# Optimization experiments

Measured on AMD Instinct MI355X. Metric: run time of the kernel, lower is better.

Reference implementation:

```python
import jax, jax.numpy as jnp
import numpy as np

N_ENT = 50000
N_REL = 200
DIM = 128
N_BASES = 4
NUM_RELATIONS = 2 * N_REL  # RGCNConv num_relations
E = 200000
S = 20000


def rgcn_conv(x, edge_index, edge_type, edge_norm, basis, att, root, bias, n_nodes):
    """RGCNConv with basis decomposition, aggr='mean'.
    x: [N, Din]; basis: [B, Din, Dout]; att: [R, B]; root: [Din, Dout]; bias: [Dout].
    """
    src, dst = edge_index[0], edge_index[1]
    x_j = x[src]                      # [E, Din] gather
    att_e = att[edge_type]            # [E, B]
    # message: x_j @ (att_e @ basis) without materializing per-edge [Din,Dout] weights
    msg = jnp.einsum('ei,bio,eb->eo', x_j, basis, att_e)  # [E, Dout]
    msg = msg * edge_norm[:, None]
    agg = jax.ops.segment_sum(msg, dst, num_segments=n_nodes)            # [N, Dout]
    cnt = jax.ops.segment_sum(jnp.ones_like(edge_norm), dst, num_segments=n_nodes)
    agg = agg / jnp.maximum(cnt, 1.0)[:, None]            # mean aggregation
    return agg + x @ root + bias


def setup_inputs() -> dict:
    key = jax.random.key(0)
    ks = jax.random.split(key, 20)
    d = {}
    d['entity'] = jnp.arange(N_ENT, dtype=jnp.int64) if jax.config.read('jax_enable_x64') else jnp.arange(N_ENT, dtype=jnp.int32)
    d['edge_index'] = jax.random.randint(ks[0], (2, E), 0, N_ENT)
    d['edge_type'] = jax.random.randint(ks[1], (E,), 0, NUM_RELATIONS)
    d['edge_norm'] = jax.random.uniform(ks[2], (E,), dtype=jnp.float32)
    d['samples'] = jax.random.randint(ks[3], (S, 3), 0, N_REL)
    d['DAD_rel'] = jax.random.normal(ks[4], (N_REL, N_REL), dtype=jnp.float32) * 0.05
    # learned parameters
    d['entity_emb'] = jax.random.normal(ks[5], (N_ENT, DIM), dtype=jnp.float32) * 0.02
    d['relation_emb'] = jax.random.normal(ks[6], (N_REL, DIM), dtype=jnp.float32) * 0.02
    d['entity_context_tab'] = jax.random.normal(ks[7], (N_ENT, DIM), dtype=jnp.float32) * 0.02
    d['relation_context_tab'] = jax.random.normal(ks[8], (N_REL, DIM), dtype=jnp.float32) * 0.02
    d['relation_gcn_weight'] = jax.random.normal(ks[9], (DIM, DIM), dtype=jnp.float32) * 0.02
    d['gate_entity'] = jax.random.uniform(ks[10], (DIM,), dtype=jnp.float32)
    d['gate_relation'] = jax.random.uniform(ks[11], (DIM,), dtype=jnp.float32)
    d['basis1'] = jax.random.normal(ks[12], (N_BASES, DIM, DIM), dtype=jnp.float32) * 0.02
    d['att1'] = jax.random.normal(ks[13], (NUM_RELATIONS, N_BASES), dtype=jnp.float32) * 0.1
    d['root1'] = jax.random.normal(ks[14], (DIM, DIM), dtype=jnp.float32) * 0.02
    d['bias1'] = jnp.zeros((DIM,), dtype=jnp.float32)
    d['basis2'] = jax.random.normal(ks[15], (N_BASES, DIM, DIM), dtype=jnp.float32) * 0.02
    d['att2'] = jax.random.normal(ks[16], (NUM_RELATIONS, N_BASES), dtype=jnp.float32) * 0.1
    d['root2'] = jax.random.normal(ks[17], (DIM, DIM), dtype=jnp.float32) * 0.02
    d['bias2'] = jnp.zeros((DIM,), dtype=jnp.float32)
    return d


def reference(entity, edge_index, edge_type, edge_norm, samples, DAD_rel,
              entity_emb, relation_emb, entity_context_tab, relation_context_tab,
              relation_gcn_weight, gate_entity, gate_relation,
              basis1, att1, root1, bias1, basis2, att2, root2, bias2):
    n_nodes = entity.shape[0]
    ent_ctx = entity_context_tab[entity]                  # [N, D]
    rel_ctx = relation_context_tab                        # arange over all relations -> full table
    ent_ctx = jax.nn.relu(rgcn_conv(ent_ctx, edge_index, edge_type, edge_norm,
                                    basis1, att1, root1, bias1, n_nodes))
    ent_ctx = jax.nn.relu(rgcn_conv(ent_ctx, edge_index, edge_type, edge_norm,
                                    basis2, att2, root2, bias2, n_nodes))
    rel_ctx = jax.nn.relu((DAD_rel @ rel_ctx) @ relation_gcn_weight)
    ge = jax.nn.sigmoid(gate_entity)
    gr = jax.nn.sigmoid(gate_relation)
    h, r, t = samples[:, 0], samples[:, 1], samples[:, 2]
    head_o = ge * entity_emb[h] + (1.0 - ge) * ent_ctx[h]
    rel_o = gr * relation_emb[r] + (1.0 - gr) * rel_ctx[r]
    tail_o = ge * entity_emb[t] + (1.0 - ge) * ent_ctx[t]
    return jnp.stack([head_o, rel_o, tail_o])             # [3, S, D]
```

## Files before the change

kernel.cpp:

```cpp
#include <hip/hip_runtime.h>
#include <hip/hip_bf16.h>

typedef short s8v  __attribute__((ext_vector_type(8)));
typedef float f16v __attribute__((ext_vector_type(16)));

__device__ __forceinline__ unsigned short f2bf(float x) {
    unsigned u = __float_as_uint(x);
    unsigned r = ((u >> 16) & 1u) + 0x7FFFu;
    return (unsigned short)((u + r) >> 16);
}
__device__ __forceinline__ float bf2f(unsigned short h) {
    return __uint_as_float(((unsigned)h) << 16);
}

__global__ __launch_bounds__(256) void hist_kernel(
    const int* __restrict__ edge_index, int* __restrict__ deg, int E)
{
    int e = blockIdx.x * 256 + threadIdx.x;
    if (e < E) atomicAdd(&deg[edge_index[E + e]], 1);
}

__global__ __launch_bounds__(1024) void scanA_kernel(
    const int* __restrict__ deg, int* __restrict__ row_start,
    int* __restrict__ btot, int N)
{
    __shared__ int wtot[16];
    __shared__ int woff[16];
    const int tid = threadIdx.x, lane = tid & 63, wid = tid >> 6;
    int i = blockIdx.x * 1024 + tid;
    int v = (i < N) ? deg[i] : 0;
    int x = v;
    #pragma unroll
    for (int d = 1; d < 64; d <<= 1) {
        int t = __shfl_up(x, d, 64);
        if (lane >= d) x += t;
    }
    if (lane == 63) wtot[wid] = x;
    __syncthreads();
    if (wid == 0 && lane < 16) {
        int s = wtot[lane];
        int y = s;
        #pragma unroll
        for (int d = 1; d < 16; d <<= 1) {
            int t = __shfl_up(y, d, 16);
            if (lane >= d) y += t;
        }
        woff[lane] = y - s;
        if (lane == 15) btot[blockIdx.x] = y;
    }
    __syncthreads();
    if (i < N) row_start[i] = woff[wid] + (x - v);
}

__global__ __launch_bounds__(1024) void scanC_kernel(
    int* __restrict__ row_start, int* __restrict__ cursor,
    const int* __restrict__ btot, int nB, int N)
{
    __shared__ int incl[64];
    const int tid = threadIdx.x;
    if (tid < 64) {
        int v = (tid < nB) ? btot[tid] : 0;
        int x = v;
        #pragma unroll
        for (int d = 1; d < 64; d <<= 1) {
            int t = __shfl_up(x, d, 64);
            if (tid >= d) x += t;
        }
        incl[tid] = x;
    }
    __syncthreads();
    int off = (blockIdx.x == 0) ? 0 : incl[blockIdx.x - 1];
    int i = blockIdx.x * 1024 + tid;
    if (i < N) {
        int r = row_start[i] + off;
        row_start[i] = r;
        cursor[i]    = r;
    }
    if (blockIdx.x == (unsigned)(nB - 1) && tid == 0)
        row_start[N] = incl[nB - 1];
}

__global__ __launch_bounds__(256) void mega_kernel(
    const float* __restrict__ DAD, const float* __restrict__ rtab,
    const float* __restrict__ Wrel, float* __restrict__ Rc, int NR,
    const int* __restrict__ edge_index, const int* __restrict__ edge_type,
    const float* __restrict__ edge_norm, int* __restrict__ cursor,
    const float* __restrict__ att1, const float* __restrict__ att2,
    int* __restrict__ src_s, float4* __restrict__ an1, float4* __restrict__ an2, int E,
    const float* __restrict__ tab, const int* __restrict__ entity,
    unsigned short* __restrict__ X0h, unsigned short* __restrict__ X0l, int N,
    const float* __restrict__ basis1, const float* __restrict__ root1,
    const float* __restrict__ basis2, const float* __restrict__ root2,
    unsigned short* __restrict__ Bp1h, unsigned short* __restrict__ Bp2h,
    int c1, int c2, int c3)
{
    __shared__ float smem[384];
    const int b = blockIdx.x, tid = threadIdx.x;

    if (b < c1) {
        float* part = smem;
        float* r1s  = smem + 256;
        int r = b;
        int o = tid & 127, q = tid >> 7;
        float s = 0.f;
        for (int j = q; j < NR; j += 2)
            s = fmaf(DAD[r * NR + j], rtab[j * 128 + o], s);
        part[q * 128 + o] = s;
        __syncthreads();
        if (tid < 128) r1s[tid] = part[tid] + part[128 + tid];
        __syncthreads();
        float s2 = 0.f;
        #pragma unroll 8
        for (int k = q * 64; k < q * 64 + 64; ++k)
            s2 = fmaf(r1s[k], Wrel[k * 128 + o], s2);
        part[q * 128 + o] = s2;
        __syncthreads();
        if (tid < 128)
            Rc[r * 128 + tid] = fmaxf(part[tid] + part[128 + tid], 0.f);
    } else if (b < c2) {
        int e = (b - c1) * 256 + tid;
        if (e >= E) return;
        int dst = edge_index[E + e];
        int et  = edge_type[e];
        float n = edge_norm[e];
        int pos = atomicAdd(&cursor[dst], 1);
        src_s[pos] = edge_index[e];
        float4 a1 = *(const float4*)&att1[(size_t)et * 4];
        float4 a2 = *(const float4*)&att2[(size_t)et * 4];
        an1[pos] = make_float4(n * a1.x, n * a1.y, n * a1.z, n * a1.w);
        an2[pos] = make_float4(n * a2.x, n * a2.y, n * a2.z, n * a2.w);
    } else if (b < c3) {
        int idx = (b - c2) * 256 + tid;
        int nn = idx >> 4, part = idx & 15;
        if (nn < N) {
            int src = entity[nn];
            const float4* sp = (const float4*)&tab[(size_t)src * 128 + part * 8];
            float4 v0 = sp[0], v1 = sp[1];
            float vs[8] = {v0.x, v0.y, v0.z, v0.w, v1.x, v1.y, v1.z, v1.w};
            s8v h8, l8;
            #pragma unroll
            for (int j = 0; j < 8; ++j) {
                unsigned short h = f2bf(vs[j]);
                h8[j] = (short)h;
                l8[j] = (short)f2bf(vs[j] - bf2f(h));
            }
            *(s8v*)&X0h[(size_t)nn * 128 + part * 8] = h8;
            *(s8v*)&X0l[(size_t)nn * 128 + part * 8] = l8;
        }
    } else {
        int bb = b - c3;
        int layer = bb >= 320;
        int idx = (layer ? bb - 320 : bb) * 256 + tid;
        int n = idx & 127, k = idx >> 7;
        const float* basis = layer ? basis2 : basis1;
        const float* root  = layer ? root2  : root1;
        float v = (k < 512) ? basis[((k & 3) << 14) + ((k >> 2) << 7) + n]
                            : root[((k - 512) << 7) + n];
        size_t pos = (((size_t)(k >> 3) * 128) + n) * 8 + (k & 7);
        (layer ? Bp2h : Bp1h)[pos] = f2bf(v);
    }
}

__global__ __launch_bounds__(512, 4) void layer_kernel(
    const unsigned short* __restrict__ Xh,
    const unsigned short* __restrict__ Xl,
    const int* __restrict__ row_start,
    const int* __restrict__ src_s,
    const float4* __restrict__ an,
    const unsigned short* __restrict__ Bph,
    const float* __restrict__ bias,
    unsigned short* __restrict__ Xoh,
    unsigned short* __restrict__ Xol,
    int N)
{
    __shared__ unsigned short Whi[64 * 32 * 8];

    const int tid   = threadIdx.x;
    const int node0 = blockIdx.x * 32;

    {
        const int g = tid >> 4, l = tid & 15;
        const int gn = node0 + g;
        const bool ok = gn < N;
        int s0 = ok ? row_start[gn] : 0;
        int s1 = ok ? row_start[gn + 1] : 0;
        float acc[8][4];
        #pragma unroll
        for (int d = 0; d < 8; ++d)
            #pragma unroll
            for (int c = 0; c < 4; ++c) acc[d][c] = 0.f;

        const int se = s1 - 1;
        for (int q0 = s0; q0 < s1; q0 += 4) {
            int q1 = min(q0 + 1, se);
            int q2 = min(q0 + 2, se);
            int q3 = min(q0 + 3, se);
            int sA = src_s[q0], sB = src_s[q1];
            int sC = src_s[q2], sD = src_s[q3];
            float4 aA = an[q0], aB = an[q1];
            float4 aC = an[q2], aD = an[q3];
            if (q0 + 1 > se) aB = make_float4(0.f, 0.f, 0.f, 0.f);
            if (q0 + 2 > se) aC = make_float4(0.f, 0.f, 0.f, 0.f);
            if (q0 + 3 > se) aD = make_float4(0.f, 0.f, 0.f, 0.f);
            s8v hA = *(const s8v*)&Xh[(size_t)sA * 128 + (l << 3)];
            s8v hB = *(const s8v*)&Xh[(size_t)sB * 128 + (l << 3)];
            s8v hC = *(const s8v*)&Xh[(size_t)sC * 128 + (l << 3)];
            s8v hD = *(const s8v*)&Xh[(size_t)sD * 128 + (l << 3)];
            #pragma unroll
            for (int d = 0; d < 8; ++d) {
                float xA = bf2f((unsigned short)hA[d]);
                float xB = bf2f((unsigned short)hB[d]);
                float xC = bf2f((unsigned short)hC[d]);
                float xD = bf2f((unsigned short)hD[d]);
                acc[d][0] = fmaf(aA.x, xA, fmaf(aB.x, xB, fmaf(aC.x, xC, fmaf(aD.x, xD, acc[d][0]))));
                acc[d][1] = fmaf(aA.y, xA, fmaf(aB.y, xB, fmaf(aC.y, xC, fmaf(aD.y, xD, acc[d][1]))));
                acc[d][2] = fmaf(aA.z, xA, fmaf(aB.z, xB, fmaf(aC.z, xC, fmaf(aD.z, xD, acc[d][2]))));
                acc[d][3] = fmaf(aA.w, xA, fmaf(aB.w, xB, fmaf(aC.w, xC, fmaf(aD.w, xD, acc[d][3]))));
            }
        }
        float inv = 1.0f / fmaxf((float)(s1 - s0), 1.0f);
        #pragma unroll
        for (int f = 0; f < 4; ++f) {
            int kh   = 4 * l + f;
            int slot = g ^ (kh & 31);
            s8v h8;
            #pragma unroll
            for (int j = 0; j < 4; ++j) {
                h8[j]     = (short)f2bf(acc[2 * f][j]     * inv);
                h8[4 + j] = (short)f2bf(acc[2 * f + 1][j] * inv);
            }
            *(s8v*)&Whi[(kh * 32 + slot) * 8] = h8;
        }
    }

    const int lane = tid & 63, wv = tid >> 6;
    const int m    = lane & 31;
    const int kh8  = lane >> 5;
    s8v xh[8], xl[8];
    if (tid < 256) {
        const s8v z8 = {0, 0, 0, 0, 0, 0, 0, 0};
        int gn  = node0 + m;
        bool ok = gn < N;
        size_t xbase = (size_t)(ok ? gn : 0) * 128;
        #pragma unroll
        for (int q = 0; q < 8; ++q) {
            int dk = 2 * q + kh8;
            xh[q] = *(const s8v*)&Xh[xbase + dk * 8];
            xl[q] = *(const s8v*)&Xl[xbase + dk * 8];
        }
        if (!ok) {
            #pragma unroll
            for (int q = 0; q < 8; ++q) { xh[q] = z8; xl[q] = z8; }
        }
    }
    __syncthreads();
    if (tid >= 256) return;

    const int c0 = wv << 5;

    f16v acc;
    #pragma unroll
    for (int i = 0; i < 16; ++i) acc[i] = 0.f;

    s8v Bb[2][4];
    auto khg_of = [&](int t) {
        return (t < 8) ? (64 + 2 * t + kh8) : (2 * (t - 8) + kh8);
    };
    auto loadB4 = [&](int g, int buf) {
        #pragma unroll
        for (int q = 0; q < 4; ++q) {
            int khg = khg_of(g * 4 + q);
            size_t off = ((size_t)khg * 128 + c0 + m) * 8;
            Bb[buf][q] = *(const s8v*)&Bph[off];
        }
    };
    loadB4(0, 0);

    #pragma unroll
    for (int g = 0; g < 10; ++g) {
        int buf = g & 1;
        if (g < 9) loadB4(g + 1, buf ^ 1);
        #pragma unroll
        for (int q = 0; q < 4; ++q) {
            int t = g * 4 + q;
            if (t < 8) {
                acc = __builtin_amdgcn_mfma_f32_32x32x16_bf16(xl[t], Bb[buf][q], acc, 0, 0, 0);
                acc = __builtin_amdgcn_mfma_f32_32x32x16_bf16(xh[t], Bb[buf][q], acc, 0, 0, 0);
            } else {
                int khg  = 2 * (t - 8) + kh8;
                int slot = m ^ (khg & 31);
                s8v aH = *(const s8v*)&Whi[(khg * 32 + slot) * 8];
                acc = __builtin_amdgcn_mfma_f32_32x32x16_bf16(aH, Bb[buf][q], acc, 0, 0, 0);
            }
        }
    }

    int gc = c0 + m;
    float bv = bias[gc];
    const int rbase = kh8 << 2;
    #pragma unroll
    for (int reg = 0; reg < 16; ++reg) {
        int gr = node0 + rbase + (reg & 3) + ((reg >> 2) << 3);
        if (gr < N) {
            float v = fmaxf(acc[reg] + bv, 0.f);
            unsigned short h = f2bf(v);
            Xoh[(size_t)gr * 128 + gc] = h;
            Xol[(size_t)gr * 128 + gc] = f2bf(v - bf2f(h));
        }
    }
}

__global__ __launch_bounds__(256) void output_kernel(
    const int* __restrict__ samples,
    const float* __restrict__ gate_e,
    const float* __restrict__ gate_r,
    const float* __restrict__ ent_emb,
    const float* __restrict__ rel_emb,
    const unsigned short* __restrict__ ctx2h,
    const unsigned short* __restrict__ ctx2l,
    const float* __restrict__ relctx,
    float* __restrict__ out, int S)
{
    const int p   = blockIdx.y;
    const int o   = threadIdx.x & 127;
    const int sub = threadIdx.x >> 7;
    const float g = (p == 1) ? 1.0f / (1.0f + __expf(-gate_r[o]))
                             : 1.0f / (1.0f + __expf(-gate_e[o]));
    const int s0 = blockIdx.x * 8 + sub;
    #pragma unroll
    for (int k = 0; k < 4; ++k) {
        int s = s0 + k * 2;
        if (s >= S) break;
        float v;
        if (p == 1) {
            int idx = samples[s * 3 + 1];
            v = g * rel_emb[idx * 128 + o] + (1.0f - g) * relctx[idx * 128 + o];
        } else {
            int idx = samples[s * 3 + (p == 0 ? 0 : 2)];
            float c = bf2f(ctx2h[(size_t)idx * 128 + o]) + bf2f(ctx2l[(size_t)idx * 128 + o]);
            v = g * ent_emb[(size_t)idx * 128 + o] + (1.0f - g) * c;
        }
        out[(size_t)p * S * 128 + (size_t)s * 128 + o] = v;
    }
}

extern "C" void kernel_launch(void* const* d_in, const int* in_sizes, int n_in,
                              void* d_out, int out_size, void* d_ws, size_t ws_size,
                              hipStream_t stream)
{
    const int*   entity     = (const int*)d_in[0];
    const int*   edge_index = (const int*)d_in[1];
    const int*   edge_type  = (const int*)d_in[2];
    const float* edge_norm  = (const float*)d_in[3];
    const int*   samples    = (const int*)d_in[4];
    const float* DAD        = (const float*)d_in[5];
    const float* ent_emb    = (const float*)d_in[6];
    const float* rel_emb    = (const float*)d_in[7];
    const float* ent_tab    = (const float*)d_in[8];
    const float* rel_tab    = (const float*)d_in[9];
    const float* Wrel       = (const float*)d_in[10];
    const float* gate_e     = (const float*)d_in[11];
    const float* gate_r     = (const float*)d_in[12];
    const float* basis1     = (const float*)d_in[13];
    const float* att1       = (const float*)d_in[14];
    const float* root1      = (const float*)d_in[15];
    const float* bias1      = (const float*)d_in[16];
    const float* basis2     = (const float*)d_in[17];
    const float* att2       = (const float*)d_in[18];
    const float* root2      = (const float*)d_in[19];
    const float* bias2      = (const float*)d_in[20];

    const int N  = in_sizes[0];
    const int E  = in_sizes[2];
    const int S  = in_sizes[4] / 3;
    const int NR = in_sizes[9] / 128;

    unsigned short* X0h = (unsigned short*)d_ws;
    unsigned short* X0l = X0h + (size_t)N * 128;
    unsigned short* X1h = X0l + (size_t)N * 128;
    unsigned short* X1l = X1h + (size_t)N * 128;
    float4* an1    = (float4*)(X1l + (size_t)N * 128);
    float4* an2    = an1 + (E + 4);
    float* Rc      = (float*)(an2 + (E + 4));
    int*   deg     = (int*)(Rc + (size_t)NR * 128);
    int*   rstart  = deg + N;
    int*   cursor  = rstart + N + 1;
    int*   src_s   = cursor + N;
    int*   btot    = src_s + E + 4;
    int*   boff    = btot + 64;
    uintptr_t bt   = ((uintptr_t)(boff + 64) + 15) & ~(uintptr_t)15;
    unsigned short* Bp1h = (unsigned short*)bt;
    unsigned short* Bp2h = Bp1h + 80 * 128 * 8;

    const int egrid = (E + 255) / 256;
    const int lgrid = (N + 31) / 32;
    const int nB    = (N + 1023) / 1024;
    const int x0blocks = (N * 16 + 255) / 256;
    const int c1 = NR;
    const int c2 = c1 + egrid;
    const int c3 = c2 + x0blocks;
    const int mgrid = c3 + 640;

    hipMemsetAsync(deg, 0, (size_t)N * sizeof(int), stream);
    hist_kernel<<<egrid, 256, 0, stream>>>(edge_index, deg, E);
    scanA_kernel<<<nB, 1024, 0, stream>>>(deg, rstart, btot, N);
    scanC_kernel<<<nB, 1024, 0, stream>>>(rstart, cursor, btot, nB, N);
    mega_kernel<<<mgrid, 256, 0, stream>>>(
        DAD, rel_tab, Wrel, Rc, NR,
        edge_index, edge_type, edge_norm, cursor, att1, att2, src_s, an1, an2, E,
        ent_tab, entity, X0h, X0l, N,
        basis1, root1, basis2, root2, Bp1h, Bp2h,
        c1, c2, c3);

    layer_kernel<<<lgrid, 512, 0, stream>>>(X0h, X0l, rstart, src_s, an1,
                                            Bp1h, bias1, X1h, X1l, N);
    layer_kernel<<<lgrid, 512, 0, stream>>>(X1h, X1l, rstart, src_s, an2,
                                            Bp2h, bias2, X0h, X0l, N);

    output_kernel<<<dim3((S + 7) / 8, 3), 256, 0, stream>>>(
        samples, gate_e, gate_r, ent_emb, rel_emb, X0h, X0l, Rc, (float*)d_out, S);
}
```

Baseline: 295.1 us.

## Fuse entity-context gather into layer 1 and pack per-edge records

Drops the separate pass that gathered the entity context table into bf16 hi/lo X0 buffers. The first layer now reads fp32 rows straight from the table through entity[] and splits them in registers. Per-edge src, entity id, type and norm are packed into one int4 record, replacing the src_s array and two precomputed float4 attention arrays. Attention coefficients are now looked up and multiplied per edge inside each layer, which adds small gathers and FLOPs. Layer 1 reads fp32 neighbour rows, twice the bytes of bf16, in exchange for skipping the write and read of X0.

```diff
diff --git a/kernel.cpp b/kernel.cpp
--- a/kernel.cpp
+++ b/kernel.cpp
@@ -84,15 +84,12 @@
     const float* __restrict__ DAD, const float* __restrict__ rtab,
     const float* __restrict__ Wrel, float* __restrict__ Rc, int NR,
     const int* __restrict__ edge_index, const int* __restrict__ edge_type,
-    const float* __restrict__ edge_norm, int* __restrict__ cursor,
-    const float* __restrict__ att1, const float* __restrict__ att2,
-    int* __restrict__ src_s, float4* __restrict__ an1, float4* __restrict__ an2, int E,
-    const float* __restrict__ tab, const int* __restrict__ entity,
-    unsigned short* __restrict__ X0h, unsigned short* __restrict__ X0l, int N,
+    const float* __restrict__ edge_norm, const int* __restrict__ entity,
+    int* __restrict__ cursor, int4* __restrict__ rec, int E,
     const float* __restrict__ basis1, const float* __restrict__ root1,
     const float* __restrict__ basis2, const float* __restrict__ root2,
     unsigned short* __restrict__ Bp1h, unsigned short* __restrict__ Bp2h,
-    int c1, int c2, int c3)
+    int c1, int c2)
 {
     __shared__ float smem[384];
     const int b = blockIdx.x, tid = threadIdx.x;
@@ -123,32 +120,12 @@
         int dst = edge_index[E + e];
         int et  = edge_type[e];
         float n = edge_norm[e];
+        int src = edge_index[e];
+        int ent = entity[src];
         int pos = atomicAdd(&cursor[dst], 1);
-        src_s[pos] = edge_index[e];
-        float4 a1 = *(const float4*)&att1[(size_t)et * 4];
-        float4 a2 = *(const float4*)&att2[(size_t)et * 4];
-        an1[pos] = make_float4(n * a1.x, n * a1.y, n * a1.z, n * a1.w);
-        an2[pos] = make_float4(n * a2.x, n * a2.y, n * a2.z, n * a2.w);
-    } else if (b < c3) {
-        int idx = (b - c2) * 256 + tid;
-        int nn = idx >> 4, part = idx & 15;
-        if (nn < N) {
-            int src = entity[nn];
-            const float4* sp = (const float4*)&tab[(size_t)src * 128 + part * 8];
-            float4 v0 = sp[0], v1 = sp[1];
-            float vs[8] = {v0.x, v0.y, v0.z, v0.w, v1.x, v1.y, v1.z, v1.w};
-            s8v h8, l8;
-            #pragma unroll
-            for (int j = 0; j < 8; ++j) {
-                unsigned short h = f2bf(vs[j]);
-                h8[j] = (short)h;
-                l8[j] = (short)f2bf(vs[j] - bf2f(h));
-            }
-            *(s8v*)&X0h[(size_t)nn * 128 + part * 8] = h8;
-            *(s8v*)&X0l[(size_t)nn * 128 + part * 8] = l8;
-        }
+        rec[pos] = make_int4(src, ent, et, __float_as_int(n));
     } else {
-        int bb = b - c3;
+        int bb = b - c2;
         int layer = bb >= 320;
         int idx = (layer ? bb - 320 : bb) * 256 + tid;
         int n = idx & 127, k = idx >> 7;
@@ -161,12 +138,15 @@
     }
 }
 
+template<bool F32SRC>
 __global__ __launch_bounds__(512, 4) void layer_kernel(
     const unsigned short* __restrict__ Xh,
     const unsigned short* __restrict__ Xl,
+    const float* __restrict__ Xf,
+    const int* __restrict__ entity,
     const int* __restrict__ row_start,
-    const int* __restrict__ src_s,
-    const float4* __restrict__ an,
+    const int4* __restrict__ rec,
+    const float* __restrict__ att,
     const unsigned short* __restrict__ Bph,
     const float* __restrict__ bias,
     unsigned short* __restrict__ Xoh,
@@ -195,27 +175,58 @@
             int q1 = min(q0 + 1, se);
             int q2 = min(q0 + 2, se);
             int q3 = min(q0 + 3, se);
-            int sA = src_s[q0], sB = src_s[q1];
-            int sC = src_s[q2], sD = src_s[q3];
-            float4 aA = an[q0], aB = an[q1];
-            float4 aC = an[q2], aD = an[q3];
-            if (q0 + 1 > se) aB = make_float4(0.f, 0.f, 0.f, 0.f);
-            if (q0 + 2 > se) aC = make_float4(0.f, 0.f, 0.f, 0.f);
-            if (q0 + 3 > se) aD = make_float4(0.f, 0.f, 0.f, 0.f);
-            s8v hA = *(const s8v*)&Xh[(size_t)sA * 128 + (l << 3)];
-            s8v hB = *(const s8v*)&Xh[(size_t)sB * 128 + (l << 3)];
-            s8v hC = *(const s8v*)&Xh[(size_t)sC * 128 + (l << 3)];
-            s8v hD = *(const s8v*)&Xh[(size_t)sD * 128 + (l << 3)];
+            int4 rA = rec[q0], rB = rec[q1], rC = rec[q2], rD = rec[q3];
+            float4 tA = *(const float4*)&att[(size_t)rA.z * 4];
+            float4 tB = *(const float4*)&att[(size_t)rB.z * 4];
+            float4 tC = *(const float4*)&att[(size_t)rC.z * 4];
+            float4 tD = *(const float4*)&att[(size_t)rD.z * 4];
+            float nA = __int_as_float(rA.w), nB_ = __int_as_float(rB.w);
+            float nC = __int_as_float(rC.w), nD = __int_as_float(rD.w);
+            if (q0 + 1 > se) nB_ = 0.f;
+            if (q0 + 2 > se) nC = 0.f;
+            if (q0 + 3 > se) nD = 0.f;
+            float4 aA = make_float4(nA * tA.x, nA * tA.y, nA * tA.z, nA * tA.w);
+            float4 aB = make_float4(nB_ * tB.x, nB_ * tB.y, nB_ * tB.z, nB_ * tB.w);
+            float4 aC = make_float4(nC * tC.x, nC * tC.y, nC * tC.z, nC * tC.w);
+            float4 aD = make_float4(nD * tD.x, nD * tD.y, nD * tD.z, nD * tD.w);
+
+            float xA[8], xB[8], xC[8], xD[8];
+            if constexpr (F32SRC) {
+                const float4* pA = (const float4*)&Xf[(size_t)rA.y * 128 + (l << 3)];
+                const float4* pB = (const float4*)&Xf[(size_t)rB.y * 128 + (l << 3)];
+                const float4* pC = (const float4*)&Xf[(size_t)rC.y * 128 + (l << 3)];
+                const float4* pD = (const float4*)&Xf[(size_t)rD.y * 128 + (l << 3)];
+                float4 uA0 = pA[0], uA1 = pA[1];
+                float4 uB0 = pB[0], uB1 = pB[1];
+                float4 uC0 = pC[0], uC1 = pC[1];
+                float4 uD0 = pD[0], uD1 = pD[1];
+                xA[0]=uA0.x; xA[1]=uA0.y; xA[2]=uA0.z; xA[3]=uA0.w;
+                xA[4]=uA1.x; xA[5]=uA1.y; xA[6]=uA1.z; xA[7]=uA1.w;
+                xB[0]=uB0.x; xB[1]=uB0.y; xB[2]=uB0.z; xB[3]=uB0.w;
+                xB[4]=uB1.x; xB[5]=uB1.y; xB[6]=uB1.z; xB[7]=uB1.w;
+                xC[0]=uC0.x; xC[1]=uC0.y; xC[2]=uC0.z; xC[3]=uC0.w;
+                xC[4]=uC1.x; xC[5]=uC1.y; xC[6]=uC1.z; xC[7]=uC1.w;
+                xD[0]=uD0.x; xD[1]=uD0.y; xD[2]=uD0.z; xD[3]=uD0.w;
+                xD[4]=uD1.x; xD[5]=uD1.y; xD[6]=uD1.z; xD[7]=uD1.w;
+            } else {
+                s8v hA = *(const s8v*)&Xh[(size_t)rA.x * 128 + (l << 3)];
+                s8v hB = *(const s8v*)&Xh[(size_t)rB.x * 128 + (l << 3)];
+                s8v hC = *(const s8v*)&Xh[(size_t)rC.x * 128 + (l << 3)];
+                s8v hD = *(const s8v*)&Xh[(size_t)rD.x * 128 + (l << 3)];
+                #pragma unroll
+                for (int d = 0; d < 8; ++d) {
+                    xA[d] = bf2f((unsigned short)hA[d]);
+                    xB[d] = bf2f((unsigned short)hB[d]);
+                    xC[d] = bf2f((unsigned short)hC[d]);
+                    xD[d] = bf2f((unsigned short)hD[d]);
+                }
+            }
             #pragma unroll
             for (int d = 0; d < 8; ++d) {
-                float xA = bf2f((unsigned short)hA[d]);
-                float xB = bf2f((unsigned short)hB[d]);
-                float xC = bf2f((unsigned short)hC[d]);
-                float xD = bf2f((unsigned short)hD[d]);
-                acc[d][0] = fmaf(aA.x, xA, fmaf(aB.x, xB, fmaf(aC.x, xC, fmaf(aD.x, xD, acc[d][0]))));
-                acc[d][1] = fmaf(aA.y, xA, fmaf(aB.y, xB, fmaf(aC.y, xC, fmaf(aD.y, xD, acc[d][1]))));
-                acc[d][2] = fmaf(aA.z, xA, fmaf(aB.z, xB, fmaf(aC.z, xC, fmaf(aD.z, xD, acc[d][2]))));
-                acc[d][3] = fmaf(aA.w, xA, fmaf(aB.w, xB, fmaf(aC.w, xC, fmaf(aD.w, xD, acc[d][3]))));
+                acc[d][0] = fmaf(aA.x, xA[d], fmaf(aB.x, xB[d], fmaf(aC.x, xC[d], fmaf(aD.x, xD[d], acc[d][0]))));
+                acc[d][1] = fmaf(aA.y, xA[d], fmaf(aB.y, xB[d], fmaf(aC.y, xC[d], fmaf(aD.y, xD[d], acc[d][1]))));
+                acc[d][2] = fmaf(aA.z, xA[d], fmaf(aB.z, xB[d], fmaf(aC.z, xC[d], fmaf(aD.z, xD[d], acc[d][2]))));
+                acc[d][3] = fmaf(aA.w, xA[d], fmaf(aB.w, xB[d], fmaf(aC.w, xC[d], fmaf(aD.w, xD[d], acc[d][3]))));
             }
         }
         float inv = 1.0f / fmaxf((float)(s1 - s0), 1.0f);
@@ -241,12 +252,32 @@
         const s8v z8 = {0, 0, 0, 0, 0, 0, 0, 0};
         int gn  = node0 + m;
         bool ok = gn < N;
-        size_t xbase = (size_t)(ok ? gn : 0) * 128;
-        #pragma unroll
-        for (int q = 0; q < 8; ++q) {
-            int dk = 2 * q + kh8;
-            xh[q] = *(const s8v*)&Xh[xbase + dk * 8];
-            xl[q] = *(const s8v*)&Xl[xbase + dk * 8];
+        if constexpr (F32SRC) {
+            int en = ok ? entity[gn] : 0;
+            const float* base = &Xf[(size_t)en * 128];
+            #pragma unroll
+            for (int q = 0; q < 8; ++q) {
+                int dk = 2 * q + kh8;
+                const float4* p = (const float4*)&base[dk * 8];
+                float4 u0 = p[0], u1 = p[1];
+                float vs[8] = {u0.x, u0.y, u0.z, u0.w, u1.x, u1.y, u1.z, u1.w};
+                s8v h8, l8;
+                #pragma unroll
+                for (int j = 0; j < 8; ++j) {
+                    unsigned short h = f2bf(vs[j]);
+                    h8[j] = (short)h;
+                    l8[j] = (short)f2bf(vs[j] - bf2f(h));
+                }
+                xh[q] = h8; xl[q] = l8;
+            }
+        } else {
+            size_t xbase = (size_t)(ok ? gn : 0) * 128;
+            #pragma unroll
+            for (int q = 0; q < 8; ++q) {
+                int dk = 2 * q + kh8;
+                xh[q] = *(const s8v*)&Xh[xbase + dk * 8];
+                xl[q] = *(const s8v*)&Xl[xbase + dk * 8];
+            }
         }
         if (!ok) {
             #pragma unroll
@@ -375,31 +406,26 @@
     const int S  = in_sizes[4] / 3;
     const int NR = in_sizes[9] / 128;
 
-    unsigned short* X0h = (unsigned short*)d_ws;
-    unsigned short* X0l = X0h + (size_t)N * 128;
-    unsigned short* X1h = X0l + (size_t)N * 128;
+    unsigned short* X1h = (unsigned short*)d_ws;
     unsigned short* X1l = X1h + (size_t)N * 128;
-    float4* an1    = (float4*)(X1l + (size_t)N * 128);
-    float4* an2    = an1 + (E + 4);
-    float* Rc      = (float*)(an2 + (E + 4));
+    unsigned short* C2h = X1l + (size_t)N * 128;
+    unsigned short* C2l = C2h + (size_t)N * 128;
+    int4*  rec     = (int4*)(C2l + (size_t)N * 128);
+    float* Rc      = (float*)(rec + (E + 4));
     int*   deg     = (int*)(Rc + (size_t)NR * 128);
     int*   rstart  = deg + N;
     int*   cursor  = rstart + N + 1;
-    int*   src_s   = cursor + N;
-    int*   btot    = src_s + E + 4;
-    int*   boff    = btot + 64;
-    uintptr_t bt   = ((uintptr_t)(boff + 64) + 15) & ~(uintptr_t)15;
+    int*   btot    = cursor + N;
+    uintptr_t bt   = ((uintptr_t)(btot + 64) + 15) & ~(uintptr_t)15;
     unsigned short* Bp1h = (unsigned short*)bt;
     unsigned short* Bp2h = Bp1h + 80 * 128 * 8;
 
     const int egrid = (E + 255) / 256;
     const int lgrid = (N + 31) / 32;
     const int nB    = (N + 1023) / 1024;
-    const int x0blocks = (N * 16 + 255) / 256;
     const int c1 = NR;
     const int c2 = c1 + egrid;
-    const int c3 = c2 + x0blocks;
-    const int mgrid = c3 + 640;
+    const int mgrid = c2 + 640;
 
     hipMemsetAsync(deg, 0, (size_t)N * sizeof(int), stream);
     hist_kernel<<<egrid, 256, 0, stream>>>(edge_index, deg, E);
@@ -407,16 +433,17 @@
     scanC_kernel<<<nB, 1024, 0, stream>>>(rstart, cursor, btot, nB, N);
     mega_kernel<<<mgrid, 256, 0, stream>>>(
         DAD, rel_tab, Wrel, Rc, NR,
-        edge_index, edge_type, edge_norm, cursor, att1, att2, src_s, an1, an2, E,
-        ent_tab, entity, X0h, X0l, N,
+        edge_index, edge_type, edge_norm, entity, cursor, rec, E,
         basis1, root1, basis2, root2, Bp1h, Bp2h,
-        c1, c2, c3);
-
-    layer_kernel<<<lgrid, 512, 0, stream>>>(X0h, X0l, rstart, src_s, an1,
-                                            Bp1h, bias1, X1h, X1l, N);
-    layer_kernel<<<lgrid, 512, 0, stream>>>(X1h, X1l, rstart, src_s, an2,
-                                            Bp2h, bias2, X0h, X0l, N);
+        c1, c2);
+
+    layer_kernel<true><<<lgrid, 512, 0, stream>>>(
+        nullptr, nullptr, ent_tab, entity, rstart, rec, att1,
+        Bp1h, bias1, X1h, X1l, N);
+    layer_kernel<false><<<lgrid, 512, 0, stream>>>(
+        X1h, X1l, nullptr, nullptr, rstart, rec, att2,
+        Bp2h, bias2, C2h, C2l, N);
 
     output_kernel<<<dim3((S + 7) / 8, 3), 256, 0, stream>>>(
-        samples, gate_e, gate_r, ent_emb, rel_emb, X0h, X0l, Rc, (float*)d_out, S);
-}
+        samples, gate_e, gate_r, ent_emb, rel_emb, C2h, C2l, Rc, (float*)d_out, S);
+}
```

Result: slower. 315.3 us (+6.9%).

## Pack edge records into int4 and compute attention weights on the fly; change LDS swizzle

Applied to the files above, without the earlier changes.

The edge scatter now writes one int4 record (src, type, norm) per edge instead of a src array plus two per-layer float4 attention arrays. Each layer kernel gathers the tiny att table by edge type and multiplies by the norm itself. This cuts scatter write traffic and workspace, at the cost of an extra dependent load per edge in the aggregation loop. The LDS slot swizzle for the staged aggregate tile also changes from an XOR to an additive rotation, aimed at avoiding bank conflicts.

```diff
diff --git a/kernel.cpp b/kernel.cpp
--- a/kernel.cpp
+++ b/kernel.cpp
@@ -84,9 +84,8 @@
     const float* __restrict__ DAD, const float* __restrict__ rtab,
     const float* __restrict__ Wrel, float* __restrict__ Rc, int NR,
     const int* __restrict__ edge_index, const int* __restrict__ edge_type,
-    const float* __restrict__ edge_norm, int* __restrict__ cursor,
-    const float* __restrict__ att1, const float* __restrict__ att2,
-    int* __restrict__ src_s, float4* __restrict__ an1, float4* __restrict__ an2, int E,
+    const float* __restrict__ edge_norm,
+    int* __restrict__ cursor, int4* __restrict__ rec, int E,
     const float* __restrict__ tab, const int* __restrict__ entity,
     unsigned short* __restrict__ X0h, unsigned short* __restrict__ X0l, int N,
     const float* __restrict__ basis1, const float* __restrict__ root1,
@@ -123,12 +122,9 @@
         int dst = edge_index[E + e];
         int et  = edge_type[e];
         float n = edge_norm[e];
+        int src = edge_index[e];
         int pos = atomicAdd(&cursor[dst], 1);
-        src_s[pos] = edge_index[e];
-        float4 a1 = *(const float4*)&att1[(size_t)et * 4];
-        float4 a2 = *(const float4*)&att2[(size_t)et * 4];
-        an1[pos] = make_float4(n * a1.x, n * a1.y, n * a1.z, n * a1.w);
-        an2[pos] = make_float4(n * a2.x, n * a2.y, n * a2.z, n * a2.w);
+        rec[pos] = make_int4(src, et, __float_as_int(n), 0);
     } else if (b < c3) {
         int idx = (b - c2) * 256 + tid;
         int nn = idx >> 4, part = idx & 15;
@@ -161,12 +157,16 @@
     }
 }
 
+__device__ __forceinline__ int wslot(int n, int kh) {
+    return (n + (kh >> 2) + ((kh & 3) << 3)) & 31;
+}
+
 __global__ __launch_bounds__(512, 4) void layer_kernel(
     const unsigned short* __restrict__ Xh,
     const unsigned short* __restrict__ Xl,
     const int* __restrict__ row_start,
-    const int* __restrict__ src_s,
-    const float4* __restrict__ an,
+    const int4* __restrict__ rec,
+    const float* __restrict__ att,
     const unsigned short* __restrict__ Bph,
     const float* __restrict__ bias,
     unsigned short* __restrict__ Xoh,
@@ -195,17 +195,24 @@
             int q1 = min(q0 + 1, se);
             int q2 = min(q0 + 2, se);
             int q3 = min(q0 + 3, se);
-            int sA = src_s[q0], sB = src_s[q1];
-            int sC = src_s[q2], sD = src_s[q3];
-            float4 aA = an[q0], aB = an[q1];
-            float4 aC = an[q2], aD = an[q3];
-            if (q0 + 1 > se) aB = make_float4(0.f, 0.f, 0.f, 0.f);
-            if (q0 + 2 > se) aC = make_float4(0.f, 0.f, 0.f, 0.f);
-            if (q0 + 3 > se) aD = make_float4(0.f, 0.f, 0.f, 0.f);
-            s8v hA = *(const s8v*)&Xh[(size_t)sA * 128 + (l << 3)];
-            s8v hB = *(const s8v*)&Xh[(size_t)sB * 128 + (l << 3)];
-            s8v hC = *(const s8v*)&Xh[(size_t)sC * 128 + (l << 3)];
-            s8v hD = *(const s8v*)&Xh[(size_t)sD * 128 + (l << 3)];
+            int4 rA = rec[q0], rB = rec[q1], rC = rec[q2], rD = rec[q3];
+            float4 tA = *(const float4*)&att[(size_t)rA.y * 4];
+            float4 tB = *(const float4*)&att[(size_t)rB.y * 4];
+            float4 tC = *(const float4*)&att[(size_t)rC.y * 4];
+            float4 tD = *(const float4*)&att[(size_t)rD.y * 4];
+            float nA = __int_as_float(rA.z), nB_ = __int_as_float(rB.z);
+            float nC = __int_as_float(rC.z), nD = __int_as_float(rD.z);
+            if (q0 + 1 > se) nB_ = 0.f;
+            if (q0 + 2 > se) nC = 0.f;
+            if (q0 + 3 > se) nD = 0.f;
+            float4 aA = make_float4(nA * tA.x, nA * tA.y, nA * tA.z, nA * tA.w);
+            float4 aB = make_float4(nB_ * tB.x, nB_ * tB.y, nB_ * tB.z, nB_ * tB.w);
+            float4 aC = make_float4(nC * tC.x, nC * tC.y, nC * tC.z, nC * tC.w);
+            float4 aD = make_float4(nD * tD.x, nD * tD.y, nD * tD.z, nD * tD.w);
+            s8v hA = *(const s8v*)&Xh[(size_t)rA.x * 128 + (l << 3)];
+            s8v hB = *(const s8v*)&Xh[(size_t)rB.x * 128 + (l << 3)];
+            s8v hC = *(const s8v*)&Xh[(size_t)rC.x * 128 + (l << 3)];
+            s8v hD = *(const s8v*)&Xh[(size_t)rD.x * 128 + (l << 3)];
             #pragma unroll
             for (int d = 0; d < 8; ++d) {
                 float xA = bf2f((unsigned short)hA[d]);
@@ -222,7 +229,7 @@
         #pragma unroll
         for (int f = 0; f < 4; ++f) {
             int kh   = 4 * l + f;
-            int slot = g ^ (kh & 31);
+            int slot = wslot(g, kh);
             s8v h8;
             #pragma unroll
             for (int j = 0; j < 4; ++j) {
@@ -288,7 +295,7 @@
                 acc = __builtin_amdgcn_mfma_f32_32x32x16_bf16(xh[t], Bb[buf][q], acc, 0, 0, 0);
             } else {
                 int khg  = 2 * (t - 8) + kh8;
-                int slot = m ^ (khg & 31);
+                int slot = wslot(m, khg);
                 s8v aH = *(const s8v*)&Whi[(khg * 32 + slot) * 8];
                 acc = __builtin_amdgcn_mfma_f32_32x32x16_bf16(aH, Bb[buf][q], acc, 0, 0, 0);
             }
@@ -379,16 +386,13 @@
     unsigned short* X0l = X0h + (size_t)N * 128;
     unsigned short* X1h = X0l + (size_t)N * 128;
     unsigned short* X1l = X1h + (size_t)N * 128;
-    float4* an1    = (float4*)(X1l + (size_t)N * 128);
-    float4* an2    = an1 + (E + 4);
-    float* Rc      = (float*)(an2 + (E + 4));
+    int4*  rec     = (int4*)(X1l + (size_t)N * 128);
+    float* Rc      = (float*)(rec + (E + 4));
     int*   deg     = (int*)(Rc + (size_t)NR * 128);
     int*   rstart  = deg + N;
     int*   cursor  = rstart + N + 1;
-    int*   src_s   = cursor + N;
-    int*   btot    = src_s + E + 4;
-    int*   boff    = btot + 64;
-    uintptr_t bt   = ((uintptr_t)(boff + 64) + 15) & ~(uintptr_t)15;
+    int*   btot    = cursor + N;
+    uintptr_t bt   = ((uintptr_t)(btot + 64) + 15) & ~(uintptr_t)15;
     unsigned short* Bp1h = (unsigned short*)bt;
     unsigned short* Bp2h = Bp1h + 80 * 128 * 8;
 
@@ -407,14 +411,14 @@
     scanC_kernel<<<nB, 1024, 0, stream>>>(rstart, cursor, btot, nB, N);
     mega_kernel<<<mgrid, 256, 0, stream>>>(
         DAD, rel_tab, Wrel, Rc, NR,
-        edge_index, edge_type, edge_norm, cursor, att1, att2, src_s, an1, an2, E,
+        edge_index, edge_type, edge_norm, cursor, rec, E,
         ent_tab, entity, X0h, X0l, N,
         basis1, root1, basis2, root2, Bp1h, Bp2h,
         c1, c2, c3);
 
-    layer_kernel<<<lgrid, 512, 0, stream>>>(X0h, X0l, rstart, src_s, an1,
+    layer_kernel<<<lgrid, 512, 0, stream>>>(X0h, X0l, rstart, rec, att1,
                                             Bp1h, bias1, X1h, X1l, N);
-    layer_kernel<<<lgrid, 512, 0, stream>>>(X1h, X1l, rstart, src_s, an2,
+    layer_kernel<<<lgrid, 512, 0, stream>>>(X1h, X1l, rstart, rec, att2,
                                             Bp2h, bias2, X0h, X0l, N);
 
     output_kernel<<<dim3((S + 7) / 8, 3), 256, 0, stream>>>(
```

Measured after the change: 289.9 us. About the same (-1.7%).
